# Performance work log

Measured on AMD Instinct MI355X. Metric: run time of the kernel, lower is better.

Reference implementation:

```python
import jax, jax.numpy as jnp
import numpy as np

N = 1024
N_FEAT = 512
HID = 256
N_KERNEL = 10
KERNEL_DIM = 10
MB_DIM = N_KERNEL * KERNEL_DIM  # 100
CAT = HID + N_KERNEL  # concat width per block
EPS = 1e-3  # keras LayerNormalization default epsilon
ALPHA = 0.3  # keras LeakyReLU default


def setup_inputs() -> dict:
    key = jax.random.key(0)
    ks = jax.random.split(key, 16)
    def w(k, shape, std=0.1):
        return (jax.random.normal(k, shape, dtype=jnp.float32) * std)
    return {
        "x": jax.random.normal(ks[0], (N, N_FEAT), dtype=jnp.float32),
        # block 0
        "W0": w(ks[1], (N_FEAT, HID)), "b0": jnp.zeros((HID,), jnp.float32),
        "Wd0": w(ks[2], (HID, MB_DIM)), "bd0": jnp.zeros((MB_DIM,), jnp.float32),
        "beta0": jnp.zeros((CAT,), jnp.float32),
        # block 1 (input width = HID + N_KERNEL)
        "W1": w(ks[3], (CAT, HID)), "b1": jnp.zeros((HID,), jnp.float32),
        "Wd1": w(ks[4], (HID, MB_DIM)), "bd1": jnp.zeros((MB_DIM,), jnp.float32),
        "beta1": jnp.zeros((CAT,), jnp.float32),
        # final critic head
        "Wf": w(ks[5], (CAT, 1)), "bf": jnp.zeros((1,), jnp.float32),
    }


def _batch_diversity(M):
    # M: [N, n_kernel*kernel_dim] -> [N, n_kernel]
    M = M.reshape(-1, N_KERNEL, KERNEL_DIM)
    # pairwise L1 distance over kernel_dim: [N, N, n_kernel]
    l1 = jnp.abs(M[:, None, :, :] - M[None, :, :, :]).sum(axis=3)
    return jnp.exp(-l1).sum(axis=0)  # [N, n_kernel]


def _layer_norm_center_only(h, beta):
    mu = h.mean(axis=-1, keepdims=True)
    var = h.var(axis=-1, keepdims=True)
    return (h - mu) * jax.lax.rsqrt(var + EPS) + beta


def _block(x, W, b, Wd, bd, beta):
    h = x @ W + b                       # [N, HID]
    div = _batch_diversity(h @ Wd + bd)  # [N, N_KERNEL]
    h = jnp.concatenate([h, div], axis=1)  # [N, CAT]
    h = _layer_norm_center_only(h, beta)   # dropout is identity at inference
    return jax.nn.leaky_relu(h, ALPHA)


def reference(x, W0, b0, Wd0, bd0, beta0, W1, b1, Wd1, bd1, beta1, Wf, bf):
    h = _block(x, W0, b0, Wd0, bd0, beta0)
    h = _block(h, W1, b1, Wd1, bd1, beta1)
    return h @ Wf + bf  # [N, 1] critic value (WGGP: no sigmoid)
```

## Files before the change

### kernel.cpp

```cpp
#include <hip/hip_runtime.h>

typedef __attribute__((ext_vector_type(8))) short short8;
typedef __attribute__((ext_vector_type(4))) float f32x4;

#define EPS   1e-3f
#define ALPHA 0.3f

#define MFMA(a, b, c) __builtin_amdgcn_mfma_f32_16x16x32_bf16((a), (b), (c), 0, 0, 0)

__device__ __forceinline__ unsigned short f2bf(float f) {
    unsigned u = __float_as_uint(f);
    unsigned r = u + 0x7FFFu + ((u >> 16) & 1u);
    return (unsigned short)(r >> 16);
}
__device__ __forceinline__ float lrelu(float v) { return v > 0.f ? v : ALPHA * v; }

__global__ __launch_bounds__(256) void prep_kernel(
    const float* __restrict__ W0, const float* __restrict__ Wd0,
    const float* __restrict__ W1, const float* __restrict__ Wd1,
    const float* __restrict__ b0, const float* __restrict__ bd0,
    const float* __restrict__ b1, const float* __restrict__ bd1,
    unsigned short* __restrict__ Wc0bT, unsigned short* __restrict__ Wc1bT,
    float* __restrict__ bcomb0, float* __restrict__ bcomb1)
{
    const int bid = blockIdx.x, t = threadIdx.x;
    if (bid < 100) {
        __shared__ unsigned short Ab[32][264];
        __shared__ unsigned short BbT[32][264];
        const float *Wsrc, *Wdsrc;
        unsigned short* Cdst;
        int ldc, ft, ct, arows;
        if (bid < 64) { ft = bid & 15; ct = bid >> 4; Wsrc = W0; Wdsrc = Wd0;
                        Cdst = Wc0bT; ldc = 512; arows = 512; }
        else { const int s = bid - 64; ft = s % 9; ct = s / 9;
               Wsrc = W1; Wdsrc = Wd1; Cdst = Wc1bT; ldc = 296; arows = 266; }

        {
            const int row = t >> 3, kc = t & 7;
            const int f = ft * 32 + row;
            if (f < arows) {
                const float* wp = Wsrc + (size_t)f * 256 + kc * 32;
#pragma unroll
                for (int i = 0; i < 8; ++i) {
                    const float4 v = ((const float4*)wp)[i];
                    Ab[row][kc * 32 + i * 4 + 0] = f2bf(v.x);
                    Ab[row][kc * 32 + i * 4 + 1] = f2bf(v.y);
                    Ab[row][kc * 32 + i * 4 + 2] = f2bf(v.z);
                    Ab[row][kc * 32 + i * 4 + 3] = f2bf(v.w);
                }
            } else {
#pragma unroll
                for (int i = 0; i < 8; ++i)
                    *(ushort4*)&Ab[row][kc * 32 + i * 4] = make_ushort4(0, 0, 0, 0);
            }
        }
        for (int idx = t; idx < 2048; idx += 256) {
            const int h = idx >> 3, c4 = idx & 7;
            const int cbase = ct * 32 + c4 * 4;
            float v[4];
            if (cbase + 3 < 100) {
                const float4 q = *(const float4*)&Wdsrc[(size_t)h * 100 + cbase];
                v[0] = q.x; v[1] = q.y; v[2] = q.z; v[3] = q.w;
            } else {
#pragma unroll
                for (int j = 0; j < 4; ++j)
                    v[j] = (cbase + j < 100) ? Wdsrc[(size_t)h * 100 + cbase + j] : 0.f;
            }
#pragma unroll
            for (int j = 0; j < 4; ++j) BbT[c4 * 4 + j][h] = f2bf(v[j]);
        }
        __syncthreads();

        const int lane = t & 63, w = t >> 6;
        const int cr = w & 1, fr = w >> 1, r = lane & 15, g = lane >> 4;
        const unsigned short* Ap = &BbT[cr * 16 + r][g * 8];
        const unsigned short* Bp = &Ab[fr * 16 + r][g * 8];
        f32x4 a0 = {0.f, 0.f, 0.f, 0.f}, a1 = {0.f, 0.f, 0.f, 0.f};
#pragma unroll
        for (int k0 = 0; k0 < 256; k0 += 64) {
            a0 = MFMA(*(const short8*)(Ap + k0),      *(const short8*)(Bp + k0),      a0);
            a1 = MFMA(*(const short8*)(Ap + k0 + 32), *(const short8*)(Bp + k0 + 32), a1);
        }
        const f32x4 acc = a0 + a1;
        const int crow = ct * 32 + cr * 16 + g * 4;
        const int fcol = ft * 32 + fr * 16 + r;
#pragma unroll
        for (int i = 0; i < 4; ++i)
            Cdst[(size_t)(crow + i) * ldc + fcol] = f2bf(acc[i]);
    } else {
        const float* bb = (bid == 100) ? b0 : b1;
        const float* Wd = (bid == 100) ? Wd0 : Wd1;
        const float* bd = (bid == 100) ? bd0 : bd1;
        float* o = (bid == 100) ? bcomb0 : bcomb1;
        if (t < 128) {
            float s = 0.f;
            if (t < 100) {
                s = bd[t];
                float s0 = 0.f, s1 = 0.f, s2 = 0.f, s3 = 0.f;
                for (int k = 0; k < 256; k += 4) {
                    s0 += bb[k]     * Wd[k * 100 + t];
                    s1 += bb[k + 1] * Wd[(k + 1) * 100 + t];
                    s2 += bb[k + 2] * Wd[(k + 2) * 100 + t];
                    s3 += bb[k + 3] * Wd[(k + 3) * 100 + t];
                }
                s += (s0 + s1) + (s2 + s3);
            }
            o[t] = s;
        }
    }
}

__global__ __launch_bounds__(256) void hm0_mfma(
    const float* __restrict__ x, const float* __restrict__ W0,
    const unsigned short* __restrict__ Wc0bT,
    const float* __restrict__ b0, const float* __restrict__ bcomb0,
    float* __restrict__ h0, float* __restrict__ Mt0)
{
    __shared__ unsigned short At[32][520];
    __shared__ unsigned short Bt[32][520];

    const int t = threadIdx.x, xt = blockIdx.x, yt = blockIdx.y;

    {
        const int row = t >> 3, kc = t & 7;
        const float* xp = x + (size_t)(xt * 32 + row) * 512 + kc * 64;
#pragma unroll
        for (int i = 0; i < 8; ++i) {
            const float4 lo = ((const float4*)xp)[i * 2];
            const float4 hi = ((const float4*)xp)[i * 2 + 1];
            short8 p;
            p[0] = f2bf(lo.x); p[1] = f2bf(lo.y); p[2] = f2bf(lo.z); p[3] = f2bf(lo.w);
            p[4] = f2bf(hi.x); p[5] = f2bf(hi.y); p[6] = f2bf(hi.z); p[7] = f2bf(hi.w);
            *(short8*)&At[row][kc * 64 + i * 8] = p;
        }
    }
    if (yt < 8) {
        const int kc = t >> 5, n = t & 31, col0 = yt * 32;
        for (int kk = 0; kk < 64; kk += 2) {
            const int k = kc * 64 + kk;
            const float a = W0[(size_t)k * 256 + col0 + n];
            const float b = W0[(size_t)(k + 1) * 256 + col0 + n];
            const unsigned pk = (unsigned)f2bf(a) | ((unsigned)f2bf(b) << 16);
            *(unsigned*)&Bt[n][k] = pk;
        }
    } else {
        const int c = t >> 3, kc = t & 7;
        const unsigned short* bp = Wc0bT + (size_t)((yt - 8) * 32 + c) * 512 + kc * 64;
#pragma unroll
        for (int i = 0; i < 8; ++i)
            *(short8*)&Bt[c][kc * 64 + i * 8] = ((const short8*)bp)[i];
    }
    __syncthreads();

    const int lane = t & 63, w = t >> 6;
    const int wr = w >> 1, wn = w & 1, r = lane & 15, g = lane >> 4;
    const int lrA = wr * 16 + r, lrB = wn * 16 + r;
    f32x4 a0 = {0.f, 0.f, 0.f, 0.f}, a1 = {0.f, 0.f, 0.f, 0.f};
#pragma unroll
    for (int k0 = 0; k0 < 512; k0 += 64) {
        a0 = MFMA(*(const short8*)&At[lrA][k0 + g * 8],
                  *(const short8*)&Bt[lrB][k0 + g * 8], a0);
        a1 = MFMA(*(const short8*)&At[lrA][k0 + 32 + g * 8],
                  *(const short8*)&Bt[lrB][k0 + 32 + g * 8], a1);
    }
    const f32x4 acc = a0 + a1;
    const int orow0 = xt * 32 + wr * 16 + g * 4;

    if (yt < 8) {
        const int bcol = yt * 32 + wn * 16 + r;
        const float bv = b0[bcol];
#pragma unroll
        for (int i = 0; i < 4; ++i)
            h0[(size_t)(orow0 + i) * 256 + bcol] = acc[i] + bv;
    } else {
        const int c = (yt - 8) * 32 + wn * 16 + r;
        if (c < 100) {
            const int kq = c / 10, d = c - kq * 10;
            const float bv = bcomb0[c];
            float* dst = Mt0 + (size_t)kq * (1024 * 16) + (size_t)orow0 * 16 + d;
#pragma unroll
            for (int i = 0; i < 4; ++i) dst[i * 16] = acc[i] + bv;
        }
    }
}

__global__ __launch_bounds__(256) void hm1_mfma(
    const unsigned short* __restrict__ a0b, const float* __restrict__ W1,
    const unsigned short* __restrict__ Wc1bT,
    const float* __restrict__ b1, const float* __restrict__ bcomb1,
    float* __restrict__ h1, float* __restrict__ Mt1)
{
    __shared__ unsigned short At[32][296];
    __shared__ unsigned short Bt[32][296];

    const int t = threadIdx.x, xt = blockIdx.x, yt = blockIdx.y;

    {
        const int row = t >> 3, kc = t & 7;
        const unsigned short* ap = a0b + (size_t)(xt * 32 + row) * 296;
        for (int i = kc; i < 37; i += 8)
            *(short8*)&At[row][i * 8] = ((const short8*)ap)[i];
    }
    if (yt < 8) {
        const int kc = t >> 5, n = t & 31, col0 = yt * 32;
        const int kkEnd = (kc == 7) ? 44 : 36;
        for (int kk = 0; kk < kkEnd; kk += 2) {
            const int k = kc * 36 + kk;
            const float a = (k < 266)     ? W1[(size_t)k * 256 + col0 + n] : 0.f;
            const float b = (k + 1 < 266) ? W1[(size_t)(k + 1) * 256 + col0 + n] : 0.f;
            const unsigned pk = (unsigned)f2bf(a) | ((unsigned)f2bf(b) << 16);
            *(unsigned*)&Bt[n][k] = pk;
        }
    } else {
        const int c = t >> 3, kc = t & 7;
        const unsigned short* bp = Wc1bT + (size_t)((yt - 8) * 32 + c) * 296;
        for (int i = kc; i < 37; i += 8)
            *(short8*)&Bt[c][i * 8] = ((const short8*)bp)[i];
    }
    __syncthreads();

    const int lane = t & 63, w = t >> 6;
    const int wr = w >> 1, wn = w & 1, r = lane & 15, g = lane >> 4;
    const int lrA = wr * 16 + r, lrB = wn * 16 + r;
    f32x4 a0 = {0.f, 0.f, 0.f, 0.f}, a1 = {0.f, 0.f, 0.f, 0.f};
#pragma unroll
    for (int k0 = 0; k0 < 256; k0 += 64) {
        a0 = MFMA(*(const short8*)&At[lrA][k0 + g * 8],
                  *(const short8*)&Bt[lrB][k0 + g * 8], a0);
        a1 = MFMA(*(const short8*)&At[lrA][k0 + 32 + g * 8],
                  *(const short8*)&Bt[lrB][k0 + 32 + g * 8], a1);
    }
    a0 = MFMA(*(const short8*)&At[lrA][256 + g * 8],
              *(const short8*)&Bt[lrB][256 + g * 8], a0);
    const f32x4 acc = a0 + a1;
    const int orow0 = xt * 32 + wr * 16 + g * 4;

    if (yt < 8) {
        const int bcol = yt * 32 + wn * 16 + r;
        const float bv = b1[bcol];
#pragma unroll
        for (int i = 0; i < 4; ++i)
            h1[(size_t)(orow0 + i) * 256 + bcol] = acc[i] + bv;
    } else {
        const int c = (yt - 8) * 32 + wn * 16 + r;
        if (c < 100) {
            const int kq = c / 10, d = c - kq * 10;
            const float bv = bcomb1[c];
            float* dst = Mt1 + (size_t)kq * (1024 * 16) + (size_t)orow0 * 16 + d;
#pragma unroll
            for (int i = 0; i < 4; ++i) dst[i * 16] = acc[i] + bv;
        }
    }
}

__global__ __launch_bounds__(256) void diversity_kernel(
    const float* __restrict__ Mt, float* __restrict__ divOut)
{
    __shared__ float Ms[1024 * 16];
    __shared__ float red[256];

    const int t = threadIdx.x;
    const float* src = Mt + (size_t)blockIdx.y * (1024 * 16);
    for (int i = t; i < 1024 * 4; i += 256)
        ((float4*)Ms)[i] = ((const float4*)src)[i];
    __syncthreads();

    const int il = t & 31, jc = t >> 5;
    const int i = blockIdx.x * 32 + il;

    const float4 m0 = *(const float4*)&Ms[i * 16];
    const float4 m1 = *(const float4*)&Ms[i * 16 + 4];
    const float2 m2 = *(const float2*)&Ms[i * 16 + 8];

    float acc = 0.f;
    const int jB = jc * 128;
#pragma unroll 2
    for (int j = jB; j < jB + 128; ++j) {
        const float4 v0 = *(const float4*)&Ms[j * 16];
        const float4 v1 = *(const float4*)&Ms[j * 16 + 4];
        const float2 v2 = *(const float2*)&Ms[j * 16 + 8];
        float l1 = fabsf(m0.x - v0.x) + fabsf(m0.y - v0.y)
                 + fabsf(m0.z - v0.z) + fabsf(m0.w - v0.w)
                 + fabsf(m1.x - v1.x) + fabsf(m1.y - v1.y)
                 + fabsf(m1.z - v1.z) + fabsf(m1.w - v1.w)
                 + fabsf(m2.x - v2.x) + fabsf(m2.y - v2.y);
        acc += __expf(-l1);
    }

    red[t] = acc;
    __syncthreads();
    if (t < 32) {
        float s = 0.f;
#pragma unroll
        for (int c = 0; c < 8; ++c) s += red[c * 32 + t];
        divOut[(size_t)(blockIdx.x * 32 + t) * 10 + blockIdx.y] = s;
    }
}

__global__ __launch_bounds__(256) void ln0_kernel(
    const float* __restrict__ h0, const float* __restrict__ div0,
    const float* __restrict__ beta0, unsigned short* __restrict__ a0b)
{
    const int t = threadIdx.x, lane = t & 63;
    const int row = blockIdx.x * 4 + (t >> 6);

    const float4 hv = ((const float4*)(h0 + (size_t)row * 256))[lane];
    const float dv = (lane < 10) ? div0[(size_t)row * 10 + lane] : 0.f;

    float s = hv.x + hv.y + hv.z + hv.w + dv;
    float q = hv.x * hv.x + hv.y * hv.y + hv.z * hv.z + hv.w * hv.w + dv * dv;
#pragma unroll
    for (int m = 32; m > 0; m >>= 1) { s += __shfl_xor(s, m); q += __shfl_xor(q, m); }

    const float mean = s * (1.f / 266.f);
    const float var  = q * (1.f / 266.f) - mean * mean;
    const float inv  = rsqrtf(var + EPS);

    const float4 bv = ((const float4*)beta0)[lane];
    ushort4 o;
    o.x = f2bf(lrelu((hv.x - mean) * inv + bv.x));
    o.y = f2bf(lrelu((hv.y - mean) * inv + bv.y));
    o.z = f2bf(lrelu((hv.z - mean) * inv + bv.z));
    o.w = f2bf(lrelu((hv.w - mean) * inv + bv.w));
    *(ushort4*)&a0b[(size_t)row * 296 + lane * 4] = o;

    if (lane < 10)
        a0b[(size_t)row * 296 + 256 + lane] = f2bf(lrelu((dv - mean) * inv + beta0[256 + lane]));
    else if (lane >= 16 && lane < 46)
        a0b[(size_t)row * 296 + 250 + lane] = 0;
}

__global__ __launch_bounds__(256) void ln_final(
    const float* __restrict__ h1, const float* __restrict__ div1,
    const float* __restrict__ beta1, const float* __restrict__ Wf,
    const float* __restrict__ bf, float* __restrict__ out)
{
    const int t = threadIdx.x, lane = t & 63;
    const int row = blockIdx.x * 4 + (t >> 6);

    const float4 hv = ((const float4*)(h1 + (size_t)row * 256))[lane];
    const float dv = (lane < 10) ? div1[(size_t)row * 10 + lane] : 0.f;

    float s = hv.x + hv.y + hv.z + hv.w + dv;
    float q = hv.x * hv.x + hv.y * hv.y + hv.z * hv.z + hv.w * hv.w + dv * dv;
#pragma unroll
    for (int m = 32; m > 0; m >>= 1) { s += __shfl_xor(s, m); q += __shfl_xor(q, m); }

    const float mean = s * (1.f / 266.f);
    const float var  = q * (1.f / 266.f) - mean * mean;
    const float inv  = rsqrtf(var + EPS);

    const float4 bv = ((const float4*)beta1)[lane];
    const float4 wf = ((const float4*)Wf)[lane];
    float d = lrelu((hv.x - mean) * inv + bv.x) * wf.x
            + lrelu((hv.y - mean) * inv + bv.y) * wf.y
            + lrelu((hv.z - mean) * inv + bv.z) * wf.z
            + lrelu((hv.w - mean) * inv + bv.w) * wf.w;
    if (lane < 10)
        d += lrelu((dv - mean) * inv + beta1[256 + lane]) * Wf[256 + lane];
#pragma unroll
    for (int m = 32; m > 0; m >>= 1) d += __shfl_xor(d, m);
    if (lane == 0) out[row] = d + bf[0];
}

extern "C" void kernel_launch(void* const* d_in, const int* in_sizes, int n_in,
                              void* d_out, int out_size, void* d_ws, size_t ws_size,
                              hipStream_t stream)
{
    const float* x     = (const float*)d_in[0];
    const float* W0    = (const float*)d_in[1];
    const float* b0    = (const float*)d_in[2];
    const float* Wd0   = (const float*)d_in[3];
    const float* bd0   = (const float*)d_in[4];
    const float* beta0 = (const float*)d_in[5];
    const float* W1    = (const float*)d_in[6];
    const float* b1    = (const float*)d_in[7];
    const float* Wd1   = (const float*)d_in[8];
    const float* bd1   = (const float*)d_in[9];
    const float* beta1 = (const float*)d_in[10];
    const float* Wf    = (const float*)d_in[11];
    const float* bf    = (const float*)d_in[12];
    float* out = (float*)d_out;

    float* fws = (float*)d_ws;
    float* h0     = fws;
    float* h1     = h0 + 1024 * 256;
    float* Mt0    = h1 + 1024 * 256;
    float* Mt1    = Mt0 + 10 * 1024 * 16;
    float* div0   = Mt1 + 10 * 1024 * 16;
    float* div1   = div0 + 1024 * 10;
    float* bcomb0 = div1 + 1024 * 10;
    float* bcomb1 = bcomb0 + 128;
    unsigned short* Wc0bT = (unsigned short*)(bcomb1 + 128);
    unsigned short* Wc1bT = Wc0bT + 128 * 512;
    unsigned short* a0b   = Wc1bT + 128 * 296;

    dim3 blk(256);

    prep_kernel<<<dim3(102), blk, 0, stream>>>(
        W0, Wd0, W1, Wd1, b0, bd0, b1, bd1, Wc0bT, Wc1bT, bcomb0, bcomb1);

    hm0_mfma<<<dim3(32, 12), blk, 0, stream>>>(
        x, W0, Wc0bT, b0, bcomb0, h0, Mt0);

    diversity_kernel<<<dim3(32, 10), blk, 0, stream>>>(Mt0, div0);

    ln0_kernel<<<dim3(256), blk, 0, stream>>>(h0, div0, beta0, a0b);

    hm1_mfma<<<dim3(32, 12), blk, 0, stream>>>(
        a0b, W1, Wc1bT, b1, bcomb1, h1, Mt1);

    diversity_kernel<<<dim3(32, 10), blk, 0, stream>>>(Mt1, div1);

    ln_final<<<dim3(256), blk, 0, stream>>>(h1, div1, beta1, Wf, bf, out);
}
```

Measured before the change: 68.98 us.

## Fuse weight-composition prep into GEMM kernels, removing separate prep launch

```diff
diff --git a/kernel.cpp b/kernel.cpp
--- a/kernel.cpp
+++ b/kernel.cpp
@@ -13,113 +13,76 @@
     unsigned r = u + 0x7FFFu + ((u >> 16) & 1u);
     return (unsigned short)(r >> 16);
 }
+__device__ __forceinline__ float bf2f(unsigned short u) {
+    return __uint_as_float((unsigned)u << 16);
+}
 __device__ __forceinline__ float lrelu(float v) { return v > 0.f ? v : ALPHA * v; }
-
-__global__ __launch_bounds__(256) void prep_kernel(
-    const float* __restrict__ W0, const float* __restrict__ Wd0,
-    const float* __restrict__ W1, const float* __restrict__ Wd1,
-    const float* __restrict__ b0, const float* __restrict__ bd0,
-    const float* __restrict__ b1, const float* __restrict__ bd1,
-    unsigned short* __restrict__ Wc0bT, unsigned short* __restrict__ Wc1bT,
-    float* __restrict__ bcomb0, float* __restrict__ bcomb1)
-{
-    const int bid = blockIdx.x, t = threadIdx.x;
-    if (bid < 100) {
-        __shared__ unsigned short Ab[32][264];
-        __shared__ unsigned short BbT[32][264];
-        const float *Wsrc, *Wdsrc;
-        unsigned short* Cdst;
-        int ldc, ft, ct, arows;
-        if (bid < 64) { ft = bid & 15; ct = bid >> 4; Wsrc = W0; Wdsrc = Wd0;
-                        Cdst = Wc0bT; ldc = 512; arows = 512; }
-        else { const int s = bid - 64; ft = s % 9; ct = s / 9;
-               Wsrc = W1; Wdsrc = Wd1; Cdst = Wc1bT; ldc = 296; arows = 266; }
-
-        {
-            const int row = t >> 3, kc = t & 7;
-            const int f = ft * 32 + row;
-            if (f < arows) {
-                const float* wp = Wsrc + (size_t)f * 256 + kc * 32;
-#pragma unroll
-                for (int i = 0; i < 8; ++i) {
-                    const float4 v = ((const float4*)wp)[i];
-                    Ab[row][kc * 32 + i * 4 + 0] = f2bf(v.x);
-                    Ab[row][kc * 32 + i * 4 + 1] = f2bf(v.y);
-                    Ab[row][kc * 32 + i * 4 + 2] = f2bf(v.z);
-                    Ab[row][kc * 32 + i * 4 + 3] = f2bf(v.w);
-                }
-            } else {
-#pragma unroll
-                for (int i = 0; i < 8; ++i)
-                    *(ushort4*)&Ab[row][kc * 32 + i * 4] = make_ushort4(0, 0, 0, 0);
-            }
-        }
-        for (int idx = t; idx < 2048; idx += 256) {
-            const int h = idx >> 3, c4 = idx & 7;
-            const int cbase = ct * 32 + c4 * 4;
-            float v[4];
-            if (cbase + 3 < 100) {
-                const float4 q = *(const float4*)&Wdsrc[(size_t)h * 100 + cbase];
-                v[0] = q.x; v[1] = q.y; v[2] = q.z; v[3] = q.w;
-            } else {
-#pragma unroll
-                for (int j = 0; j < 4; ++j)
-                    v[j] = (cbase + j < 100) ? Wdsrc[(size_t)h * 100 + cbase + j] : 0.f;
-            }
-#pragma unroll
-            for (int j = 0; j < 4; ++j) BbT[c4 * 4 + j][h] = f2bf(v[j]);
-        }
-        __syncthreads();
-
-        const int lane = t & 63, w = t >> 6;
-        const int cr = w & 1, fr = w >> 1, r = lane & 15, g = lane >> 4;
-        const unsigned short* Ap = &BbT[cr * 16 + r][g * 8];
-        const unsigned short* Bp = &Ab[fr * 16 + r][g * 8];
-        f32x4 a0 = {0.f, 0.f, 0.f, 0.f}, a1 = {0.f, 0.f, 0.f, 0.f};
-#pragma unroll
-        for (int k0 = 0; k0 < 256; k0 += 64) {
-            a0 = MFMA(*(const short8*)(Ap + k0),      *(const short8*)(Bp + k0),      a0);
-            a1 = MFMA(*(const short8*)(Ap + k0 + 32), *(const short8*)(Bp + k0 + 32), a1);
-        }
-        const f32x4 acc = a0 + a1;
-        const int crow = ct * 32 + cr * 16 + g * 4;
-        const int fcol = ft * 32 + fr * 16 + r;
-#pragma unroll
-        for (int i = 0; i < 4; ++i)
-            Cdst[(size_t)(crow + i) * ldc + fcol] = f2bf(acc[i]);
-    } else {
-        const float* bb = (bid == 100) ? b0 : b1;
-        const float* Wd = (bid == 100) ? Wd0 : Wd1;
-        const float* bd = (bid == 100) ? bd0 : bd1;
-        float* o = (bid == 100) ? bcomb0 : bcomb1;
-        if (t < 128) {
-            float s = 0.f;
-            if (t < 100) {
-                s = bd[t];
-                float s0 = 0.f, s1 = 0.f, s2 = 0.f, s3 = 0.f;
-                for (int k = 0; k < 256; k += 4) {
-                    s0 += bb[k]     * Wd[k * 100 + t];
-                    s1 += bb[k + 1] * Wd[(k + 1) * 100 + t];
-                    s2 += bb[k + 2] * Wd[(k + 2) * 100 + t];
-                    s3 += bb[k + 3] * Wd[(k + 3) * 100 + t];
-                }
-                s += (s0 + s1) + (s2 + s3);
-            }
-            o[t] = s;
-        }
-    }
-}
 
 __global__ __launch_bounds__(256) void hm0_mfma(
     const float* __restrict__ x, const float* __restrict__ W0,
-    const unsigned short* __restrict__ Wc0bT,
-    const float* __restrict__ b0, const float* __restrict__ bcomb0,
+    const float* __restrict__ b0,
+    const float* __restrict__ Wd0, const float* __restrict__ bd0,
     float* __restrict__ h0, float* __restrict__ Mt0)
 {
     __shared__ unsigned short At[32][520];
     __shared__ unsigned short Bt[32][520];
+    __shared__ float bt8[8][32];
+    __shared__ float bcomb[32];
 
     const int t = threadIdx.x, xt = blockIdx.x, yt = blockIdx.y;
+    const int lane = t & 63, w = t >> 6;
+    const int r = lane & 15, g = lane >> 4;
+
+    if (yt >= 8) {
+        const int ct = yt - 8;
+        unsigned short (*WdTs)[264] = (unsigned short(*)[264])&At[0][0];
+        for (int idx = t; idx < 8192; idx += 256) {
+            const int h = idx >> 5, c = idx & 31;
+            const int cg = ct * 32 + c;
+            WdTs[c][h] = (cg < 100) ? f2bf(Wd0[(size_t)h * 100 + cg])
+                                    : (unsigned short)0;
+        }
+        __syncthreads();
+        {
+            const int c = t & 31, hc = t >> 5;
+            float s = 0.f;
+#pragma unroll
+            for (int hh = 0; hh < 32; ++hh)
+                s += b0[hc * 32 + hh] * bf2f(WdTs[c][hc * 32 + hh]);
+            bt8[hc][c] = s;
+        }
+        for (int f8 = 0; f8 < 8; ++f8) {
+            const int fr = w * 8 + f8;
+            const float* wrow = W0 + (size_t)(fr * 16 + r) * 256 + g * 8;
+            f32x4 c0 = {0.f, 0.f, 0.f, 0.f}, c1 = {0.f, 0.f, 0.f, 0.f};
+#pragma unroll
+            for (int k0 = 0; k0 < 256; k0 += 32) {
+                const float4 u = *(const float4*)(wrow + k0);
+                const float4 v = *(const float4*)(wrow + k0 + 4);
+                short8 bfr;
+                bfr[0] = f2bf(u.x); bfr[1] = f2bf(u.y);
+                bfr[2] = f2bf(u.z); bfr[3] = f2bf(u.w);
+                bfr[4] = f2bf(v.x); bfr[5] = f2bf(v.y);
+                bfr[6] = f2bf(v.z); bfr[7] = f2bf(v.w);
+                c0 = MFMA(*(const short8*)&WdTs[r][k0 + g * 8],      bfr, c0);
+                c1 = MFMA(*(const short8*)&WdTs[16 + r][k0 + g * 8], bfr, c1);
+            }
+            const int fcol = fr * 16 + r;
+#pragma unroll
+            for (int i = 0; i < 4; ++i) {
+                Bt[g * 4 + i][fcol]      = f2bf(c0[i]);
+                Bt[16 + g * 4 + i][fcol] = f2bf(c1[i]);
+            }
+        }
+        __syncthreads();
+        if (t < 32) {
+            const int cg = ct * 32 + t;
+            float s = (cg < 100) ? bd0[cg] : 0.f;
+#pragma unroll
+            for (int j = 0; j < 8; ++j) s += bt8[j][t];
+            bcomb[t] = s;
+        }
+    }
 
     {
         const int row = t >> 3, kc = t & 7;
@@ -140,20 +103,12 @@
             const int k = kc * 64 + kk;
             const float a = W0[(size_t)k * 256 + col0 + n];
             const float b = W0[(size_t)(k + 1) * 256 + col0 + n];
-            const unsigned pk = (unsigned)f2bf(a) | ((unsigned)f2bf(b) << 16);
-            *(unsigned*)&Bt[n][k] = pk;
-        }
-    } else {
-        const int c = t >> 3, kc = t & 7;
-        const unsigned short* bp = Wc0bT + (size_t)((yt - 8) * 32 + c) * 512 + kc * 64;
-#pragma unroll
-        for (int i = 0; i < 8; ++i)
-            *(short8*)&Bt[c][kc * 64 + i * 8] = ((const short8*)bp)[i];
+            *(unsigned*)&Bt[n][k] = (unsigned)f2bf(a) | ((unsigned)f2bf(b) << 16);
+        }
     }
     __syncthreads();
 
-    const int lane = t & 63, w = t >> 6;
-    const int wr = w >> 1, wn = w & 1, r = lane & 15, g = lane >> 4;
+    const int wr = w >> 1, wn = w & 1;
     const int lrA = wr * 16 + r, lrB = wn * 16 + r;
     f32x4 a0 = {0.f, 0.f, 0.f, 0.f}, a1 = {0.f, 0.f, 0.f, 0.f};
 #pragma unroll
@@ -173,10 +128,11 @@
         for (int i = 0; i < 4; ++i)
             h0[(size_t)(orow0 + i) * 256 + bcol] = acc[i] + bv;
     } else {
-        const int c = (yt - 8) * 32 + wn * 16 + r;
+        const int cl = wn * 16 + r;
+        const int c = (yt - 8) * 32 + cl;
         if (c < 100) {
             const int kq = c / 10, d = c - kq * 10;
-            const float bv = bcomb0[c];
+            const float bv = bcomb[cl];
             float* dst = Mt0 + (size_t)kq * (1024 * 16) + (size_t)orow0 * 16 + d;
 #pragma unroll
             for (int i = 0; i < 4; ++i) dst[i * 16] = acc[i] + bv;
@@ -186,14 +142,74 @@
 
 __global__ __launch_bounds__(256) void hm1_mfma(
     const unsigned short* __restrict__ a0b, const float* __restrict__ W1,
-    const unsigned short* __restrict__ Wc1bT,
-    const float* __restrict__ b1, const float* __restrict__ bcomb1,
+    const float* __restrict__ b1,
+    const float* __restrict__ Wd1, const float* __restrict__ bd1,
     float* __restrict__ h1, float* __restrict__ Mt1)
 {
     __shared__ unsigned short At[32][296];
     __shared__ unsigned short Bt[32][296];
+    __shared__ float bt8[8][32];
+    __shared__ float bcomb[32];
 
     const int t = threadIdx.x, xt = blockIdx.x, yt = blockIdx.y;
+    const int lane = t & 63, w = t >> 6;
+    const int r = lane & 15, g = lane >> 4;
+
+    if (yt >= 8) {
+        const int ct = yt - 8;
+        unsigned short (*WdTs)[264] = (unsigned short(*)[264])&At[0][0];
+        for (int idx = t; idx < 8192; idx += 256) {
+            const int h = idx >> 5, c = idx & 31;
+            const int cg = ct * 32 + c;
+            WdTs[c][h] = (cg < 100) ? f2bf(Wd1[(size_t)h * 100 + cg])
+                                    : (unsigned short)0;
+        }
+        __syncthreads();
+        {
+            const int c = t & 31, hc = t >> 5;
+            float s = 0.f;
+#pragma unroll
+            for (int hh = 0; hh < 32; ++hh)
+                s += b1[hc * 32 + hh] * bf2f(WdTs[c][hc * 32 + hh]);
+            bt8[hc][c] = s;
+        }
+        for (int f8 = 0; f8 < 5; ++f8) {
+            const int fr = f8 * 4 + w;
+            if (fr >= 18) break;
+            const int a = fr * 16 + r;
+            const float* wrow = W1 + (size_t)a * 256 + g * 8;
+            const bool live = (a < 266);
+            f32x4 c0 = {0.f, 0.f, 0.f, 0.f}, c1 = {0.f, 0.f, 0.f, 0.f};
+#pragma unroll
+            for (int k0 = 0; k0 < 256; k0 += 32) {
+                short8 bfr = {0, 0, 0, 0, 0, 0, 0, 0};
+                if (live) {
+                    const float4 u = *(const float4*)(wrow + k0);
+                    const float4 v = *(const float4*)(wrow + k0 + 4);
+                    bfr[0] = f2bf(u.x); bfr[1] = f2bf(u.y);
+                    bfr[2] = f2bf(u.z); bfr[3] = f2bf(u.w);
+                    bfr[4] = f2bf(v.x); bfr[5] = f2bf(v.y);
+                    bfr[6] = f2bf(v.z); bfr[7] = f2bf(v.w);
+                }
+                c0 = MFMA(*(const short8*)&WdTs[r][k0 + g * 8],      bfr, c0);
+                c1 = MFMA(*(const short8*)&WdTs[16 + r][k0 + g * 8], bfr, c1);
+            }
+            const int fcol = fr * 16 + r;
+#pragma unroll
+            for (int i = 0; i < 4; ++i) {
+                Bt[g * 4 + i][fcol]      = f2bf(c0[i]);
+                Bt[16 + g * 4 + i][fcol] = f2bf(c1[i]);
+            }
+        }
+        __syncthreads();
+        if (t < 32) {
+            const int cg = ct * 32 + t;
+            float s = (cg < 100) ? bd1[cg] : 0.f;
+#pragma unroll
+            for (int j = 0; j < 8; ++j) s += bt8[j][t];
+            bcomb[t] = s;
+        }
+    }
 
     {
         const int row = t >> 3, kc = t & 7;
@@ -208,19 +224,12 @@
             const int k = kc * 36 + kk;
             const float a = (k < 266)     ? W1[(size_t)k * 256 + col0 + n] : 0.f;
             const float b = (k + 1 < 266) ? W1[(size_t)(k + 1) * 256 + col0 + n] : 0.f;
-            const unsigned pk = (unsigned)f2bf(a) | ((unsigned)f2bf(b) << 16);
-            *(unsigned*)&Bt[n][k] = pk;
-        }
-    } else {
-        const int c = t >> 3, kc = t & 7;
-        const unsigned short* bp = Wc1bT + (size_t)((yt - 8) * 32 + c) * 296;
-        for (int i = kc; i < 37; i += 8)
-            *(short8*)&Bt[c][i * 8] = ((const short8*)bp)[i];
+            *(unsigned*)&Bt[n][k] = (unsigned)f2bf(a) | ((unsigned)f2bf(b) << 16);
+        }
     }
     __syncthreads();
 
-    const int lane = t & 63, w = t >> 6;
-    const int wr = w >> 1, wn = w & 1, r = lane & 15, g = lane >> 4;
+    const int wr = w >> 1, wn = w & 1;
     const int lrA = wr * 16 + r, lrB = wn * 16 + r;
     f32x4 a0 = {0.f, 0.f, 0.f, 0.f}, a1 = {0.f, 0.f, 0.f, 0.f};
 #pragma unroll
@@ -242,10 +251,11 @@
         for (int i = 0; i < 4; ++i)
             h1[(size_t)(orow0 + i) * 256 + bcol] = acc[i] + bv;
     } else {
-        const int c = (yt - 8) * 32 + wn * 16 + r;
+        const int cl = wn * 16 + r;
+        const int c = (yt - 8) * 32 + cl;
         if (c < 100) {
             const int kq = c / 10, d = c - kq * 10;
-            const float bv = bcomb1[c];
+            const float bv = bcomb[cl];
             float* dst = Mt1 + (size_t)kq * (1024 * 16) + (size_t)orow0 * 16 + d;
 #pragma unroll
             for (int i = 0; i < 4; ++i) dst[i * 16] = acc[i] + bv;
@@ -383,32 +393,23 @@
     float* out = (float*)d_out;
 
     float* fws = (float*)d_ws;
-    float* h0     = fws;
-    float* h1     = h0 + 1024 * 256;
-    float* Mt0    = h1 + 1024 * 256;
-    float* Mt1    = Mt0 + 10 * 1024 * 16;
-    float* div0   = Mt1 + 10 * 1024 * 16;
-    float* div1   = div0 + 1024 * 10;
-    float* bcomb0 = div1 + 1024 * 10;
-    float* bcomb1 = bcomb0 + 128;
-    unsigned short* Wc0bT = (unsigned short*)(bcomb1 + 128);
-    unsigned short* Wc1bT = Wc0bT + 128 * 512;
-    unsigned short* a0b   = Wc1bT + 128 * 296;
+    float* h0   = fws;
+    float* h1   = h0 + 1024 * 256;
+    float* Mt0  = h1 + 1024 * 256;
+    float* Mt1  = Mt0 + 10 * 1024 * 16;
+    float* div0 = Mt1 + 10 * 1024 * 16;
+    float* div1 = div0 + 1024 * 10;
+    unsigned short* a0b = (unsigned short*)(div1 + 1024 * 10);
 
     dim3 blk(256);
 
-    prep_kernel<<<dim3(102), blk, 0, stream>>>(
-        W0, Wd0, W1, Wd1, b0, bd0, b1, bd1, Wc0bT, Wc1bT, bcomb0, bcomb1);
-
-    hm0_mfma<<<dim3(32, 12), blk, 0, stream>>>(
-        x, W0, Wc0bT, b0, bcomb0, h0, Mt0);
+    hm0_mfma<<<dim3(32, 12), blk, 0, stream>>>(x, W0, b0, Wd0, bd0, h0, Mt0);
 
     diversity_kernel<<<dim3(32, 10), blk, 0, stream>>>(Mt0, div0);
 
     ln0_kernel<<<dim3(256), blk, 0, stream>>>(h0, div0, beta0, a0b);
 
-    hm1_mfma<<<dim3(32, 12), blk, 0, stream>>>(
-        a0b, W1, Wc1bT, b1, bcomb1, h1, Mt1);
+    hm1_mfma<<<dim3(32, 12), blk, 0, stream>>>(a0b, W1, b1, Wd1, bd1, h1, Mt1);
 
     diversity_kernel<<<dim3(32, 10), blk, 0, stream>>>(Mt1, div1);
 
```

Result: slower. 92.13 us (+33.6%).
